# Kernel optimization log

Measured on AMD Instinct MI355X. Metric: run time of the kernel, lower is better.

## Reference

```python
import jax, jax.numpy as jnp
import numpy as np

B, L, D, H = 4, 2048, 1024, 16
NEG = 1e7


def pos_encodings(length, d_model, dtype):
    d_half = d_model // 2
    pos = jnp.arange(length, dtype=dtype)
    freqs = jnp.arange(d_half, dtype=dtype)
    periods = 1.0 / (10000.0 ** (freqs / d_half))
    ang = pos[:, None] * periods[None, :]          # [L, D/2]
    # interleave: even cols = sin, odd cols = cos
    return jnp.stack([jnp.sin(ang), jnp.cos(ang)], axis=-1).reshape(length, d_model)


def setup_inputs() -> dict:
    key = jax.random.key(0)
    ks = jax.random.split(key, 12)
    s = 1.0 / np.sqrt(D)
    return {
        "q": jax.random.normal(ks[0], (B, L, D), jnp.float32),
        "k": jax.random.normal(ks[1], (B, L, D), jnp.float32),
        "v": jax.random.normal(ks[2], (B, L, D), jnp.float32),
        "padding": jnp.zeros((B, L), dtype=bool),
        "Wq": jax.random.normal(ks[3], (D, D), jnp.float32) * s,
        "bq": jax.random.normal(ks[4], (D,), jnp.float32) * s,
        "Wk": jax.random.normal(ks[5], (D, D), jnp.float32) * s,
        "bk": jax.random.normal(ks[6], (D,), jnp.float32) * s,
        "Wv": jax.random.normal(ks[7], (D, D), jnp.float32) * s,
        "bv": jax.random.normal(ks[8], (D,), jnp.float32) * s,
        "Wo": jax.random.normal(ks[9], (D, D), jnp.float32) * s,
        "bo": jax.random.normal(ks[10], (D,), jnp.float32) * s,
    }


def reference(q, k, v, padding, Wq, bq, Wk, bk, Wv, bv, Wo, bo):
    dtype = q.dtype
    d_head = D // H
    pe = pos_encodings(L, D, dtype)                # cache_index = 0

    qp = (q + pe) @ Wq + bq                        # [B, L, D]
    kp = (k + pe) @ Wk + bk
    vp = v @ Wv + bv

    # ... l (h d) -> ... h l d
    def split_heads(x):
        return x.reshape(B, L, H, d_head).transpose(0, 2, 1, 3)

    qh, kh, vh = split_heads(qp), split_heads(kp), split_heads(vp)

    scores = jnp.einsum('bhqd,bhkd->bhqk', qh, kh) * (d_head ** -0.5)

    causal = jnp.triu(jnp.ones((L, L), dtype=bool), k=1)       # [L, L]
    mask = padding[:, None, None, :] | causal                  # [B, 1, L, L]
    scores = scores - mask.astype(scores.dtype) * NEG

    out = jnp.einsum('bhqk,bhkd->bhqd', jax.nn.softmax(scores, axis=-1), vh)
    out = out.transpose(0, 2, 1, 3).reshape(B, L, D)           # ... h l d -> ... l (h d)
    return out @ Wo + bo
```

## Files before the change

### kernel.cpp

```cpp
#include <hip/hip_runtime.h>
#include <hip/hip_bf16.h>


typedef __bf16 bf16_t;
typedef bf16_t bf16x8 __attribute__((ext_vector_type(8)));
typedef bf16_t bf16x4 __attribute__((ext_vector_type(4)));
typedef float  f32x4  __attribute__((ext_vector_type(4)));

#define MFMA_16x16x32(a, b, c) __builtin_amdgcn_mfma_f32_16x16x32_bf16((a), (b), (c), 0, 0, 0)

constexpr int Lc = 2048, Dc = 1024;
constexpr int Mc = 8192;
#define QSCALE 0.18033688011112042f

__device__ __forceinline__ void gload16(const void* g, void* l) {
  __builtin_amdgcn_global_load_lds(
      (const __attribute__((address_space(1))) void*)g,
      (__attribute__((address_space(3))) void*)l, 16, 0, 0);
}

template <bool DO_V>
__global__ __launch_bounds__(256)
void qkv_prep_kernel(const float* __restrict__ q, const float* __restrict__ k,
                     const float* __restrict__ v, bf16_t* __restrict__ Aq,
                     bf16_t* __restrict__ Ak, bf16_t* __restrict__ Av) {
  int id  = blockIdx.x * 256 + threadIdx.x;
  int row = id >> 7;
  int c   = (id & 127) * 8;
  int pos = row & (Lc - 1);
  float period = __expf(-(float)(c >> 1) * 0.017988946039015984f);
  const float ratio = 0.98217189f;
  float pe8[8];
#pragma unroll
  for (int j = 0; j < 4; ++j) {
    float rev = ((float)pos * period) * 0.15915494309189535f;
    float rf = rev - floorf(rev);
    pe8[2 * j]     = __builtin_amdgcn_sinf(rf);
    pe8[2 * j + 1] = __builtin_amdgcn_cosf(rf);
    period *= ratio;
  }
  size_t off = (size_t)row * Dc + c;
  f32x4 q0 = *(const f32x4*)&q[off], q1 = *(const f32x4*)&q[off + 4];
  f32x4 k0 = *(const f32x4*)&k[off], k1 = *(const f32x4*)&k[off + 4];
  bf16x8 aq, ak;
#pragma unroll
  for (int e = 0; e < 4; ++e) {
    aq[e]     = (bf16_t)(q0[e] + pe8[e]);
    aq[4 + e] = (bf16_t)(q1[e] + pe8[4 + e]);
    ak[e]     = (bf16_t)(k0[e] + pe8[e]);
    ak[4 + e] = (bf16_t)(k1[e] + pe8[4 + e]);
  }
  *(bf16x8*)&Aq[off] = aq;
  *(bf16x8*)&Ak[off] = ak;
  if (DO_V) {
    f32x4 v0 = *(const f32x4*)&v[off], v1 = *(const f32x4*)&v[off + 4];
    bf16x8 av;
#pragma unroll
    for (int e = 0; e < 4; ++e) { av[e] = (bf16_t)v0[e]; av[4 + e] = (bf16_t)v1[e]; }
    *(bf16x8*)&Av[off] = av;
  }
}

__device__ __forceinline__ void w_prep_body(const float* W, bf16_t* Wt, int tid, int blk) {
  __shared__ float tile[64][65];
  int k0 = (blk >> 4) * 64, n0 = (blk & 15) * 64;
  int tc = tid & 63, tr = tid >> 6;
#pragma unroll
  for (int j = 0; j < 16; ++j) {
    int r = j * 4 + tr;
    tile[r][tc] = W[(size_t)(k0 + r) * Dc + n0 + tc];
  }
  __syncthreads();
#pragma unroll
  for (int j = 0; j < 16; ++j) {
    int r = j * 4 + tr;
    Wt[(size_t)(n0 + r) * Dc + k0 + tc] = (bf16_t)tile[tc][r];
  }
}

__global__ __launch_bounds__(256)
void w_prep_kernel(const float* __restrict__ W, bf16_t* __restrict__ Wt) {
  w_prep_body(W, Wt, threadIdx.x, blockIdx.x);
}

__global__ __launch_bounds__(256)
void w_prep4_kernel(const float* __restrict__ W0, const float* __restrict__ W1,
                    const float* __restrict__ W2, const float* __restrict__ W3,
                    bf16_t* __restrict__ Wt) {
  int sel = blockIdx.x >> 8;
  const float* W = (sel == 0) ? W0 : (sel == 1) ? W1 : (sel == 2) ? W2 : W3;
  w_prep_body(W, Wt + (size_t)sel * Dc * Dc, threadIdx.x, blockIdx.x & 255);
}

template <int TMODE, typename OutT, int SEGS>
__global__ __launch_bounds__(512, 4)
void gemm_db_kernel(const bf16_t* __restrict__ A0, const bf16_t* __restrict__ A1,
                    const bf16_t* __restrict__ A2,
                    const bf16_t* __restrict__ W0, const bf16_t* __restrict__ W1,
                    const bf16_t* __restrict__ W2,
                    const float* __restrict__ b0, const float* __restrict__ b1,
                    const float* __restrict__ b2,
                    OutT* __restrict__ C0, OutT* __restrict__ C1,
                    OutT* __restrict__ C2,
                    float s0, float s1, float s2) {
  constexpr int K = 1024, N = 1024, LDS_T = 136;
  __shared__ bf16_t smem[32768];
  int bid = blockIdx.x;
  int seg = (SEGS >= 2) ? (bid >> 9) : 0;
  bid &= 511;
  const bf16_t* A    = (seg == 0) ? A0 : (seg == 1) ? A1 : A2;
  const bf16_t* Wt   = (seg == 0) ? W0 : (seg == 1) ? W1 : W2;
  const float*  bias = (seg == 0) ? b0 : (seg == 1) ? b1 : b2;
  OutT*         C    = (seg == 0) ? C0 : (seg == 1) ? C1 : C2;
  float scale        = (seg == 0) ? s0 : (seg == 1) ? s1 : s2;
  bool dotrans       = (TMODE == 1) || (TMODE == 2 && seg == 2);
  int xcd = bid & 7, slot = bid >> 3;
  int m0 = (xcd * 8 + (slot >> 3)) * 128;
  int n0 = (slot & 7) * 128;
  int t = threadIdx.x, lane = t & 63, w = t >> 6;
  int l16 = lane & 15, lq = lane >> 4;
  int wm = (w >> 1) * 32, wn = (w & 1) * 64;
  int srow = lane >> 3;
  int scol = ((lane & 7) ^ srow) << 3;
  int swz = l16 & 7;
  f32x4 acc[2][4] = {};

  auto STAGE = [&](int c, int k0) {
    bf16_t* Ash = &smem[c * 16384];
    bf16_t* Bsh = Ash + 8192;
#pragma unroll
    for (int j = 0; j < 2; ++j) {
      int r8 = (w * 2 + j) * 8;
      gload16(&A[(size_t)(m0 + r8 + srow) * K + k0 + scol], &Ash[r8 * 64]);
      gload16(&Wt[(size_t)(n0 + r8 + srow) * K + k0 + scol], &Bsh[r8 * 64]);
    }
  };

  STAGE(0, 0);
  int c = 0;
#pragma unroll 1
  for (int ti = 0; ti < 16; ++ti) {
    if (ti < 15) {
      STAGE(c ^ 1, (ti + 1) * 64);
      asm volatile("s_waitcnt vmcnt(4)" ::: "memory");
    } else {
      asm volatile("s_waitcnt vmcnt(0)" ::: "memory");
    }
    __builtin_amdgcn_s_barrier();
    const bf16_t* Ash = &smem[c * 16384];
    const bf16_t* Bsh = Ash + 8192;
#pragma unroll
    for (int ks = 0; ks < 2; ++ks) {
      bf16x8 af[2], bfr[4];
#pragma unroll
      for (int mt = 0; mt < 2; ++mt)
        af[mt] = *(const bf16x8*)&Ash[(wm + mt * 16 + l16) * 64 + (((ks * 4 + lq) ^ swz) << 3)];
#pragma unroll
      for (int nt = 0; nt < 4; ++nt)
        bfr[nt] = *(const bf16x8*)&Bsh[(wn + nt * 16 + l16) * 64 + (((ks * 4 + lq) ^ swz) << 3)];
#pragma unroll
      for (int mt = 0; mt < 2; ++mt)
#pragma unroll
        for (int nt = 0; nt < 4; ++nt)
          acc[mt][nt] = MFMA_16x16x32(af[mt], bfr[nt], acc[mt][nt]);
    }
    __builtin_amdgcn_s_barrier();
    c ^= 1;
  }

  if (dotrans) {
    bf16_t* sT = smem;
#pragma unroll
    for (int nt = 0; nt < 4; ++nt) {
      float bv = bias[n0 + wn + nt * 16 + l16];
#pragma unroll
      for (int mt = 0; mt < 2; ++mt) {
        bf16x4 p4;
#pragma unroll
        for (int r = 0; r < 4; ++r) p4[r] = (bf16_t)(acc[mt][nt][r] + bv);
        *(bf16x4*)&sT[(wn + nt * 16 + l16) * LDS_T + wm + mt * 16 + lq * 4] = p4;
      }
    }
    __syncthreads();
    int b = m0 >> 11, kp0 = m0 & (Lc - 1);
#pragma unroll
    for (int i = 0; i < 4; ++i) {
      int cidx = t + i * 512;
      int coln = cidx >> 4, cc = (cidx & 15) * 8;
      *(bf16x8*)&((bf16_t*)C)[((size_t)b * 1024 + n0 + coln) * (size_t)Lc + kp0 + cc] =
          *(const bf16x8*)&sT[coln * LDS_T + cc];
    }
  } else {
#pragma unroll
    for (int nt = 0; nt < 4; ++nt) {
      float bv = bias[n0 + wn + nt * 16 + l16];
#pragma unroll
      for (int mt = 0; mt < 2; ++mt) {
        int row = m0 + wm + mt * 16 + lq * 4;
        int col = n0 + wn + nt * 16 + l16;
#pragma unroll
        for (int r = 0; r < 4; ++r)
          C[(size_t)(row + r) * N + col] = (OutT)((acc[mt][nt][r] + bv) * scale);
      }
    }
  }
}

__global__ __launch_bounds__(512, 4)
void gemm_af32_kernel(const float* __restrict__ A, const bf16_t* __restrict__ Wt,
                      const float* __restrict__ bias, bf16_t* __restrict__ C) {
  constexpr int K = 1024, LDS_T = 136;
  __shared__ bf16_t smem[17408];
  bf16_t* Ash = smem;
  bf16_t* Bsh = smem + 8192;
  int bid = blockIdx.x;
  int xcd = bid & 7, slot = bid >> 3;
  int m0 = (xcd * 8 + (slot >> 3)) * 128;
  int n0 = (slot & 7) * 128;
  int t = threadIdx.x, lane = t & 63, w = t >> 6;
  int l16 = lane & 15, lq = lane >> 4;
  int wm = (w >> 1) * 32, wn = (w & 1) * 64;
  int srow = lane >> 3;
  int scol = ((lane & 7) ^ srow) << 3;
  int swz = l16 & 7;
  f32x4 acc[2][4] = {};

  for (int k0 = 0; k0 < K; k0 += 64) {
#pragma unroll
    for (int i = 0; i < 2; ++i) {
      int id = t + i * 512;
      int row = id >> 3, cc = (id & 7) * 8;
      f32x4 a0 = *(const f32x4*)&A[(size_t)(m0 + row) * K + k0 + cc];
      f32x4 a1 = *(const f32x4*)&A[(size_t)(m0 + row) * K + k0 + cc + 4];
      bf16x8 ah;
#pragma unroll
      for (int e = 0; e < 4; ++e) { ah[e] = (bf16_t)a0[e]; ah[4 + e] = (bf16_t)a1[e]; }
      *(bf16x8*)&Ash[row * 64 + (((cc >> 3) ^ (row & 7)) << 3)] = ah;
    }
#pragma unroll
    for (int j = 0; j < 2; ++j) {
      int r8 = (w * 2 + j) * 8;
      gload16(&Wt[(size_t)(n0 + r8 + srow) * K + k0 + scol], &Bsh[r8 * 64]);
    }
    __syncthreads();
#pragma unroll
    for (int ks = 0; ks < 2; ++ks) {
      bf16x8 af[2], bfr[4];
#pragma unroll
      for (int mt = 0; mt < 2; ++mt)
        af[mt] = *(const bf16x8*)&Ash[(wm + mt * 16 + l16) * 64 + (((ks * 4 + lq) ^ swz) << 3)];
#pragma unroll
      for (int nt = 0; nt < 4; ++nt)
        bfr[nt] = *(const bf16x8*)&Bsh[(wn + nt * 16 + l16) * 64 + (((ks * 4 + lq) ^ swz) << 3)];
#pragma unroll
      for (int mt = 0; mt < 2; ++mt)
#pragma unroll
        for (int nt = 0; nt < 4; ++nt)
          acc[mt][nt] = MFMA_16x16x32(af[mt], bfr[nt], acc[mt][nt]);
    }
    __syncthreads();
  }

  bf16_t* sT = smem;
#pragma unroll
  for (int nt = 0; nt < 4; ++nt) {
    float bv = bias[n0 + wn + nt * 16 + l16];
#pragma unroll
    for (int mt = 0; mt < 2; ++mt) {
      bf16x4 p4;
#pragma unroll
      for (int r = 0; r < 4; ++r) p4[r] = (bf16_t)(acc[mt][nt][r] + bv);
      *(bf16x4*)&sT[(wn + nt * 16 + l16) * LDS_T + wm + mt * 16 + lq * 4] = p4;
    }
  }
  __syncthreads();
  int b = m0 >> 11, kp0 = m0 & (Lc - 1);
#pragma unroll
  for (int i = 0; i < 4; ++i) {
    int cidx = t + i * 512;
    int coln = cidx >> 4, cc = (cidx & 15) * 8;
    *(bf16x8*)&C[((size_t)b * 1024 + n0 + coln) * (size_t)Lc + kp0 + cc] =
        *(const bf16x8*)&sT[coln * LDS_T + cc];
  }
}

__global__ __launch_bounds__(256, 4)
void attn_kernel(const bf16_t* __restrict__ Qp, const bf16_t* __restrict__ Kp,
                 const bf16_t* __restrict__ VpT, bf16_t* __restrict__ O) {
  __shared__ bf16_t Ks[2][4096];
  __shared__ bf16_t Vt[2][4096];
  __shared__ bf16_t Ps[4096];
  int bid = blockIdx.x;
  int xcd = bid & 7, slot = bid >> 3;
  int bh = xcd * 8 + (slot >> 4);
  int px = slot & 15;
  int b = bh >> 4, h = bh & 15;
  int t = threadIdx.x, lane = t & 63, w = t >> 6;
  int l16 = lane & 15, lq = lane >> 4;
  int srow = lane >> 3;
  int scol = ((lane & 7) ^ srow) << 3;
  int swz = l16 & 7;
  const size_t base  = ((size_t)b * Lc) * Dc + h * 64;
  const size_t vbase = ((size_t)b * 1024 + h * 64) * (size_t)Lc;

  bf16x8 ones;
#pragma unroll
  for (int e = 0; e < 8; ++e) ones[e] = (bf16_t)1.0f;

  auto STAGE = [&](int cc, int kt) {
    int kbase = kt * 64;
#pragma unroll
    for (int j = 0; j < 2; ++j) {
      int r8 = (w * 2 + j) * 8;
      int row = r8 + srow;
      gload16(&Kp[base + (size_t)(kbase + row) * Dc + scol], &Ks[cc][r8 * 64]);
      gload16(&VpT[vbase + (size_t)row * Lc + kbase + scol], &Vt[cc][r8 * 64]);
    }
  };

#pragma unroll 1
  for (int phase = 0; phase < 2; ++phase) {
    int qt = phase ? 31 - px : px;
    int q0 = qt * 64;

    bf16x8 aq[2];
#pragma unroll
    for (int kd = 0; kd < 2; ++kd)
      aq[kd] = *(const bf16x8*)&Qp[base + (size_t)(q0 + w * 16 + l16) * Dc + kd * 32 + lq * 8];

    f32x4 oacc[4] = {};
    f32x4 lacc = {};
    int qrow = q0 + w * 16 + l16;

    STAGE(0, 0);
    int c = 0;
#pragma unroll 1
    for (int kt = 0; kt <= qt; ++kt) {
      if (kt < qt) {
        STAGE(c ^ 1, kt + 1);
        asm volatile("s_waitcnt vmcnt(4)" ::: "memory");
      } else {
        asm volatile("s_waitcnt vmcnt(0)" ::: "memory");
      }
      __builtin_amdgcn_s_barrier();

      int kbase = kt * 64;
      f32x4 sacc[4] = {};
#pragma unroll
      for (int ks = 0; ks < 2; ++ks) {
        bf16x8 bk[4];
#pragma unroll
        for (int nt = 0; nt < 4; ++nt)
          bk[nt] = *(const bf16x8*)&Ks[c][(nt * 16 + l16) * 64 + (((ks * 4 + lq) ^ swz) << 3)];
#pragma unroll
        for (int nt = 0; nt < 4; ++nt)
          sacc[nt] = MFMA_16x16x32(bk[nt], aq[ks], sacc[nt]);
      }

      if (kt == qt) {
#pragma unroll
        for (int nt = 0; nt < 4; ++nt)
#pragma unroll
          for (int r = 0; r < 4; ++r)
            if (kbase + nt * 16 + lq * 4 + r > qrow) sacc[nt][r] = -1.0e7f;
      }

#pragma unroll
      for (int nt = 0; nt < 4; ++nt) {
        bf16x4 p4;
#pragma unroll
        for (int r = 0; r < 4; ++r) p4[r] = (bf16_t)exp2f(sacc[nt][r]);
        int k4 = nt * 4 + lq;
        *(bf16x4*)&Ps[(w * 16 + l16) * 64 + (((k4 >> 1) ^ swz) << 3) + ((k4 & 1) << 2)] = p4;
      }

#pragma unroll
      for (int ks = 0; ks < 2; ++ks) {
        bf16x8 ap = *(const bf16x8*)&Ps[(w * 16 + l16) * 64 + (((ks * 4 + lq) ^ swz) << 3)];
        lacc = MFMA_16x16x32(ap, ones, lacc);
        bf16x8 bv[4];
#pragma unroll
        for (int nt = 0; nt < 4; ++nt)
          bv[nt] = *(const bf16x8*)&Vt[c][(nt * 16 + l16) * 64 + (((ks * 4 + lq) ^ swz) << 3)];
#pragma unroll
        for (int nt = 0; nt < 4; ++nt)
          oacc[nt] = MFMA_16x16x32(ap, bv[nt], oacc[nt]);
      }
      __builtin_amdgcn_s_barrier();
      c ^= 1;
    }

#pragma unroll
    for (int r = 0; r < 4; ++r) {
      float inv = __builtin_amdgcn_rcpf(lacc[r]);
      int row = q0 + w * 16 + lq * 4 + r;
#pragma unroll
      for (int nt = 0; nt < 4; ++nt)
        O[base + (size_t)row * Dc + nt * 16 + l16] = (bf16_t)(oacc[nt][r] * inv);
    }
  }
}

extern "C" void kernel_launch(void* const* d_in, const int* in_sizes, int n_in,
                              void* d_out, int out_size, void* d_ws, size_t ws_size,
                              hipStream_t stream) {
  (void)in_sizes; (void)n_in; (void)out_size;
  const float* q  = (const float*)d_in[0];
  const float* k  = (const float*)d_in[1];
  const float* v  = (const float*)d_in[2];
  const float* Wq = (const float*)d_in[4];
  const float* bq = (const float*)d_in[5];
  const float* Wk = (const float*)d_in[6];
  const float* bk = (const float*)d_in[7];
  const float* Wv = (const float*)d_in[8];
  const float* bv = (const float*)d_in[9];
  const float* Wo = (const float*)d_in[10];
  const float* bo = (const float*)d_in[11];
  float* out = (float*)d_out;

  char* ws = (char*)d_ws;
  constexpr size_t WT_B  = (size_t)Dc * Dc * 2;
  constexpr size_t MAT_B = (size_t)Mc * Dc * 2;
  constexpr size_t WSZ   = (size_t)Dc * Dc;

  if (ws_size >= 4 * WT_B + 6 * MAT_B) {
    bf16_t* WT  = (bf16_t*)(ws);
    bf16_t* Aq  = (bf16_t*)(ws + 4 * WT_B);
    bf16_t* Ak  = (bf16_t*)(ws + 4 * WT_B + 1 * MAT_B);
    bf16_t* Av  = (bf16_t*)(ws + 4 * WT_B + 2 * MAT_B);
    bf16_t* Qp  = (bf16_t*)(ws + 4 * WT_B + 3 * MAT_B);
    bf16_t* Kp  = (bf16_t*)(ws + 4 * WT_B + 4 * MAT_B);
    bf16_t* VpT = (bf16_t*)(ws + 4 * WT_B + 5 * MAT_B);
    bf16_t* Ob  = Qp;

    qkv_prep_kernel<true><<<4096, 256, 0, stream>>>(q, k, v, Aq, Ak, Av);
    w_prep4_kernel<<<1024, 256, 0, stream>>>(Wq, Wk, Wv, Wo, WT);
    gemm_db_kernel<2, bf16_t, 3><<<1536, 512, 0, stream>>>(
        Aq, Ak, Av, WT, WT + WSZ, WT + 2 * WSZ, bq, bk, bv,
        Qp, Kp, VpT, QSCALE, 1.0f, 1.0f);
    attn_kernel<<<1024, 256, 0, stream>>>(Qp, Kp, VpT, Ob);
    gemm_db_kernel<0, float, 1><<<512, 512, 0, stream>>>(
        Ob, Ob, Ob, WT + 3 * WSZ, WT + 3 * WSZ, WT + 3 * WSZ, bo, bo, bo,
        out, out, out, 1.0f, 1.0f, 1.0f);
  } else if (ws_size >= 4 * WT_B + 5 * MAT_B) {
    bf16_t* WT  = (bf16_t*)(ws);
    bf16_t* Aq  = (bf16_t*)(ws + 4 * WT_B);
    bf16_t* Ak  = (bf16_t*)(ws + 4 * WT_B + 1 * MAT_B);
    bf16_t* Av  = (bf16_t*)(ws + 4 * WT_B + 2 * MAT_B);
    bf16_t* Qp  = (bf16_t*)(ws + 4 * WT_B + 3 * MAT_B);
    bf16_t* Kp  = (bf16_t*)(ws + 4 * WT_B + 4 * MAT_B);
    bf16_t* VpT = Aq;
    bf16_t* Ob  = Qp;

    qkv_prep_kernel<true><<<4096, 256, 0, stream>>>(q, k, v, Aq, Ak, Av);
    w_prep4_kernel<<<1024, 256, 0, stream>>>(Wq, Wk, Wv, Wo, WT);
    gemm_db_kernel<0, bf16_t, 2><<<1024, 512, 0, stream>>>(
        Aq, Ak, Ak, WT, WT + WSZ, WT + WSZ, bq, bk, bk,
        Qp, Kp, Kp, QSCALE, 1.0f, 1.0f);
    gemm_db_kernel<1, bf16_t, 1><<<512, 512, 0, stream>>>(
        Av, Av, Av, WT + 2 * WSZ, WT + 2 * WSZ, WT + 2 * WSZ, bv, bv, bv,
        VpT, VpT, VpT, 1.0f, 1.0f, 1.0f);
    attn_kernel<<<1024, 256, 0, stream>>>(Qp, Kp, VpT, Ob);
    gemm_db_kernel<0, float, 1><<<512, 512, 0, stream>>>(
        Ob, Ob, Ob, WT + 3 * WSZ, WT + 3 * WSZ, WT + 3 * WSZ, bo, bo, bo,
        out, out, out, 1.0f, 1.0f, 1.0f);
  } else {
    bf16_t* WT  = (bf16_t*)(ws);
    bf16_t* Aq  = (bf16_t*)(ws + WT_B);
    bf16_t* Ak  = (bf16_t*)(ws + WT_B + 1 * MAT_B);
    bf16_t* Qp  = (bf16_t*)(ws + WT_B + 2 * MAT_B);
    bf16_t* Kp  = Aq;
    bf16_t* VpT = Ak;
    bf16_t* Ob  = Qp;

    qkv_prep_kernel<false><<<4096, 256, 0, stream>>>(q, k, nullptr, Aq, Ak, nullptr);

    w_prep_kernel<<<256, 256, 0, stream>>>(Wq, WT);
    gemm_db_kernel<0, bf16_t, 1><<<512, 512, 0, stream>>>(
        Aq, Aq, Aq, WT, WT, WT, bq, bq, bq, Qp, Qp, Qp, QSCALE, QSCALE, QSCALE);

    w_prep_kernel<<<256, 256, 0, stream>>>(Wk, WT);
    gemm_db_kernel<0, bf16_t, 1><<<512, 512, 0, stream>>>(
        Ak, Ak, Ak, WT, WT, WT, bk, bk, bk, Kp, Kp, Kp, 1.0f, 1.0f, 1.0f);

    w_prep_kernel<<<256, 256, 0, stream>>>(Wv, WT);
    gemm_af32_kernel<<<512, 512, 0, stream>>>(v, WT, bv, VpT);

    attn_kernel<<<1024, 256, 0, stream>>>(Qp, Kp, VpT, Ob);

    w_prep_kernel<<<256, 256, 0, stream>>>(Wo, WT);
    gemm_db_kernel<0, float, 1><<<512, 512, 0, stream>>>(
        Ob, Ob, Ob, WT, WT, WT, bo, bo, bo, out, out, out, 1.0f, 1.0f, 1.0f);
  }
}
```

Before: 312.0 us.

## Rewrite attention with 32x32 MFMA, register P via lane shuffles, fuse prep kernels

The attention kernel moves from 16x16x32 to 32x32x16 MFMA tiles. Each of two waves now owns 32 query rows, and the softmax probabilities are rearranged between the half-waves with a cross-lane shuffle instead of a round trip through shared memory, so the Ps buffer goes away. Block size drops to 128 threads, and each thread issues twice as many staging loads per tile. Separately, the activation-prep and weight-transpose kernels are merged into one launch to save a kernel launch, at the cost of fewer waves per block and larger accumulator register use in attention.

Result: slower. 324.7 us (+4.1%).

```diff
diff --git a/kernel.cpp b/kernel.cpp
--- a/kernel.cpp
+++ b/kernel.cpp
@@ -6,8 +6,10 @@
 typedef bf16_t bf16x8 __attribute__((ext_vector_type(8)));
 typedef bf16_t bf16x4 __attribute__((ext_vector_type(4)));
 typedef float  f32x4  __attribute__((ext_vector_type(4)));
+typedef float  f32x16 __attribute__((ext_vector_type(16)));
 
 #define MFMA_16x16x32(a, b, c) __builtin_amdgcn_mfma_f32_16x16x32_bf16((a), (b), (c), 0, 0, 0)
+#define MFMA_32x32x16(a, b, c) __builtin_amdgcn_mfma_f32_32x32x16_bf16((a), (b), (c), 0, 0, 0)
 
 constexpr int Lc = 2048, Dc = 1024;
 constexpr int Mc = 8192;
@@ -20,11 +22,9 @@
 }
 
 template <bool DO_V>
-__global__ __launch_bounds__(256)
-void qkv_prep_kernel(const float* __restrict__ q, const float* __restrict__ k,
-                     const float* __restrict__ v, bf16_t* __restrict__ Aq,
-                     bf16_t* __restrict__ Ak, bf16_t* __restrict__ Av) {
-  int id  = blockIdx.x * 256 + threadIdx.x;
+__device__ __forceinline__ void qkv_prep_body(
+    const float* q, const float* k, const float* v,
+    bf16_t* Aq, bf16_t* Ak, bf16_t* Av, int id) {
   int row = id >> 7;
   int c   = (id & 127) * 8;
   int pos = row & (Lc - 1);
@@ -61,6 +61,14 @@
   }
 }
 
+template <bool DO_V>
+__global__ __launch_bounds__(256)
+void qkv_prep_kernel(const float* __restrict__ q, const float* __restrict__ k,
+                     const float* __restrict__ v, bf16_t* __restrict__ Aq,
+                     bf16_t* __restrict__ Ak, bf16_t* __restrict__ Av) {
+  qkv_prep_body<DO_V>(q, k, v, Aq, Ak, Av, blockIdx.x * 256 + threadIdx.x);
+}
+
 __device__ __forceinline__ void w_prep_body(const float* W, bf16_t* Wt, int tid, int blk) {
   __shared__ float tile[64][65];
   int k0 = (blk >> 4) * 64, n0 = (blk & 15) * 64;
@@ -84,12 +92,20 @@
 }
 
 __global__ __launch_bounds__(256)
-void w_prep4_kernel(const float* __restrict__ W0, const float* __restrict__ W1,
-                    const float* __restrict__ W2, const float* __restrict__ W3,
-                    bf16_t* __restrict__ Wt) {
-  int sel = blockIdx.x >> 8;
-  const float* W = (sel == 0) ? W0 : (sel == 1) ? W1 : (sel == 2) ? W2 : W3;
-  w_prep_body(W, Wt + (size_t)sel * Dc * Dc, threadIdx.x, blockIdx.x & 255);
+void prep_fused_kernel(const float* __restrict__ q, const float* __restrict__ k,
+                       const float* __restrict__ v, bf16_t* __restrict__ Aq,
+                       bf16_t* __restrict__ Ak, bf16_t* __restrict__ Av,
+                       const float* __restrict__ W0, const float* __restrict__ W1,
+                       const float* __restrict__ W2, const float* __restrict__ W3,
+                       bf16_t* __restrict__ Wt) {
+  if (blockIdx.x >= 4096) {
+    int bb = blockIdx.x - 4096;
+    int sel = bb >> 8;
+    const float* W = (sel == 0) ? W0 : (sel == 1) ? W1 : (sel == 2) ? W2 : W3;
+    w_prep_body(W, Wt + (size_t)sel * Dc * Dc, threadIdx.x, bb & 255);
+    return;
+  }
+  qkv_prep_body<true>(q, k, v, Aq, Ak, Av, blockIdx.x * 256 + threadIdx.x);
 }
 
 template <int TMODE, typename OutT, int SEGS>
@@ -284,22 +300,20 @@
   }
 }
 
-__global__ __launch_bounds__(256, 4)
+__global__ __launch_bounds__(128, 2)
 void attn_kernel(const bf16_t* __restrict__ Qp, const bf16_t* __restrict__ Kp,
                  const bf16_t* __restrict__ VpT, bf16_t* __restrict__ O) {
   __shared__ bf16_t Ks[2][4096];
   __shared__ bf16_t Vt[2][4096];
-  __shared__ bf16_t Ps[4096];
   int bid = blockIdx.x;
   int xcd = bid & 7, slot = bid >> 3;
   int bh = xcd * 8 + (slot >> 4);
   int px = slot & 15;
   int b = bh >> 4, h = bh & 15;
   int t = threadIdx.x, lane = t & 63, w = t >> 6;
-  int l16 = lane & 15, lq = lane >> 4;
+  int l32 = lane & 31, hi = lane >> 5;
   int srow = lane >> 3;
   int scol = ((lane & 7) ^ srow) << 3;
-  int swz = l16 & 7;
   const size_t base  = ((size_t)b * Lc) * Dc + h * 64;
   const size_t vbase = ((size_t)b * 1024 + h * 64) * (size_t)Lc;
 
@@ -310,8 +324,8 @@
   auto STAGE = [&](int cc, int kt) {
     int kbase = kt * 64;
 #pragma unroll
-    for (int j = 0; j < 2; ++j) {
-      int r8 = (w * 2 + j) * 8;
+    for (int j = 0; j < 4; ++j) {
+      int r8 = (w * 4 + j) * 8;
       int row = r8 + srow;
       gload16(&Kp[base + (size_t)(kbase + row) * Dc + scol], &Ks[cc][r8 * 64]);
       gload16(&VpT[vbase + (size_t)row * Lc + kbase + scol], &Vt[cc][r8 * 64]);
@@ -322,15 +336,15 @@
   for (int phase = 0; phase < 2; ++phase) {
     int qt = phase ? 31 - px : px;
     int q0 = qt * 64;
-
-    bf16x8 aq[2];
-#pragma unroll
-    for (int kd = 0; kd < 2; ++kd)
-      aq[kd] = *(const bf16x8*)&Qp[base + (size_t)(q0 + w * 16 + l16) * Dc + kd * 32 + lq * 8];
-
-    f32x4 oacc[4] = {};
-    f32x4 lacc = {};
-    int qrow = q0 + w * 16 + l16;
+    int qrow = q0 + w * 32 + l32;
+
+    bf16x8 qf[4];
+#pragma unroll
+    for (int ds = 0; ds < 4; ++ds)
+      qf[ds] = *(const bf16x8*)&Qp[base + (size_t)qrow * Dc + ds * 16 + hi * 8];
+
+    f32x16 oacc[2] = {};
+    f32x16 lacc = {};
 
     STAGE(0, 0);
     int c = 0;
@@ -338,65 +352,82 @@
     for (int kt = 0; kt <= qt; ++kt) {
       if (kt < qt) {
         STAGE(c ^ 1, kt + 1);
-        asm volatile("s_waitcnt vmcnt(4)" ::: "memory");
+        asm volatile("s_waitcnt vmcnt(8)" ::: "memory");
       } else {
         asm volatile("s_waitcnt vmcnt(0)" ::: "memory");
       }
       __builtin_amdgcn_s_barrier();
 
+      f32x16 sacc[2] = {};
+#pragma unroll
+      for (int t32 = 0; t32 < 2; ++t32) {
+        int row = t32 * 32 + l32;
+        int rsw = (row & 7);
+#pragma unroll
+        for (int ds = 0; ds < 4; ++ds) {
+          bf16x8 kf = *(const bf16x8*)&Ks[c][row * 64 + (((ds * 2 + hi) ^ rsw) << 3)];
+          sacc[t32] = MFMA_32x32x16(kf, qf[ds], sacc[t32]);
+        }
+      }
+
       int kbase = kt * 64;
-      f32x4 sacc[4] = {};
-#pragma unroll
-      for (int ks = 0; ks < 2; ++ks) {
-        bf16x8 bk[4];
-#pragma unroll
-        for (int nt = 0; nt < 4; ++nt)
-          bk[nt] = *(const bf16x8*)&Ks[c][(nt * 16 + l16) * 64 + (((ks * 4 + lq) ^ swz) << 3)];
-#pragma unroll
-        for (int nt = 0; nt < 4; ++nt)
-          sacc[nt] = MFMA_16x16x32(bk[nt], aq[ks], sacc[nt]);
-      }
-
       if (kt == qt) {
 #pragma unroll
-        for (int nt = 0; nt < 4; ++nt)
-#pragma unroll
-          for (int r = 0; r < 4; ++r)
-            if (kbase + nt * 16 + lq * 4 + r > qrow) sacc[nt][r] = -1.0e7f;
-      }
-
-#pragma unroll
-      for (int nt = 0; nt < 4; ++nt) {
-        bf16x4 p4;
-#pragma unroll
-        for (int r = 0; r < 4; ++r) p4[r] = (bf16_t)exp2f(sacc[nt][r]);
-        int k4 = nt * 4 + lq;
-        *(bf16x4*)&Ps[(w * 16 + l16) * 64 + (((k4 >> 1) ^ swz) << 3) + ((k4 & 1) << 2)] = p4;
-      }
-
-#pragma unroll
-      for (int ks = 0; ks < 2; ++ks) {
-        bf16x8 ap = *(const bf16x8*)&Ps[(w * 16 + l16) * 64 + (((ks * 4 + lq) ^ swz) << 3)];
-        lacc = MFMA_16x16x32(ap, ones, lacc);
-        bf16x8 bv[4];
-#pragma unroll
-        for (int nt = 0; nt < 4; ++nt)
-          bv[nt] = *(const bf16x8*)&Vt[c][(nt * 16 + l16) * 64 + (((ks * 4 + lq) ^ swz) << 3)];
-#pragma unroll
-        for (int nt = 0; nt < 4; ++nt)
-          oacc[nt] = MFMA_16x16x32(ap, bv[nt], oacc[nt]);
+        for (int t32 = 0; t32 < 2; ++t32)
+#pragma unroll
+          for (int r = 0; r < 16; ++r) {
+            int kpos = kbase + t32 * 32 + (r & 3) + 8 * (r >> 2) + 4 * hi;
+            if (kpos > qrow) sacc[t32][r] = -1.0e7f;
+          }
+      }
+
+      bf16x4 pown[8];
+#pragma unroll
+      for (int t32 = 0; t32 < 2; ++t32)
+#pragma unroll
+        for (int g2 = 0; g2 < 4; ++g2) {
+          bf16x4 g;
+#pragma unroll
+          for (int r4 = 0; r4 < 4; ++r4) g[r4] = (bf16_t)exp2f(sacc[t32][g2 * 4 + r4]);
+          pown[t32 * 4 + g2] = g;
+        }
+
+      bf16x8 pa[4];
+#pragma unroll
+      for (int s = 0; s < 4; ++s) {
+        bf16x4 sendg = hi ? pown[2 * s] : pown[2 * s + 1];
+        unsigned long long sv = __builtin_bit_cast(unsigned long long, sendg);
+        unsigned long long rv = __shfl_xor(sv, 32);
+        bf16x4 rg = __builtin_bit_cast(bf16x4, rv);
+        bf16x4 glo = hi ? rg : pown[2 * s];
+        bf16x4 ghi = hi ? pown[2 * s + 1] : rg;
+        bf16x8 f;
+#pragma unroll
+        for (int e = 0; e < 4; ++e) { f[e] = glo[e]; f[4 + e] = ghi[e]; }
+        pa[s] = f;
+      }
+
+#pragma unroll
+      for (int s = 0; s < 4; ++s) {
+        lacc = MFMA_32x32x16(pa[s], ones, lacc);
+#pragma unroll
+        for (int dt = 0; dt < 2; ++dt) {
+          int row = dt * 32 + l32;
+          bf16x8 vf = *(const bf16x8*)&Vt[c][row * 64 + (((s * 2 + hi) ^ (row & 7)) << 3)];
+          oacc[dt] = MFMA_32x32x16(pa[s], vf, oacc[dt]);
+        }
       }
       __builtin_amdgcn_s_barrier();
       c ^= 1;
     }
 
 #pragma unroll
-    for (int r = 0; r < 4; ++r) {
+    for (int r = 0; r < 16; ++r) {
       float inv = __builtin_amdgcn_rcpf(lacc[r]);
-      int row = q0 + w * 16 + lq * 4 + r;
-#pragma unroll
-      for (int nt = 0; nt < 4; ++nt)
-        O[base + (size_t)row * Dc + nt * 16 + l16] = (bf16_t)(oacc[nt][r] * inv);
+      int qr = q0 + w * 32 + (r & 3) + 8 * (r >> 2) + 4 * hi;
+#pragma unroll
+      for (int dt = 0; dt < 2; ++dt)
+        O[base + (size_t)qr * Dc + dt * 32 + l32] = (bf16_t)(oacc[dt][r] * inv);
     }
   }
 }
@@ -433,12 +464,12 @@
     bf16_t* VpT = (bf16_t*)(ws + 4 * WT_B + 5 * MAT_B);
     bf16_t* Ob  = Qp;
 
-    qkv_prep_kernel<true><<<4096, 256, 0, stream>>>(q, k, v, Aq, Ak, Av);
-    w_prep4_kernel<<<1024, 256, 0, stream>>>(Wq, Wk, Wv, Wo, WT);
+    prep_fused_kernel<<<5120, 256, 0, stream>>>(q, k, v, Aq, Ak, Av,
+                                                Wq, Wk, Wv, Wo, WT);
     gemm_db_kernel<2, bf16_t, 3><<<1536, 512, 0, stream>>>(
         Aq, Ak, Av, WT, WT + WSZ, WT + 2 * WSZ, bq, bk, bv,
         Qp, Kp, VpT, QSCALE, 1.0f, 1.0f);
-    attn_kernel<<<1024, 256, 0, stream>>>(Qp, Kp, VpT, Ob);
+    attn_kernel<<<1024, 128, 0, stream>>>(Qp, Kp, VpT, Ob);
     gemm_db_kernel<0, float, 1><<<512, 512, 0, stream>>>(
         Ob, Ob, Ob, WT + 3 * WSZ, WT + 3 * WSZ, WT + 3 * WSZ, bo, bo, bo,
         out, out, out, 1.0f, 1.0f, 1.0f);
@@ -452,15 +483,15 @@
     bf16_t* VpT = Aq;
     bf16_t* Ob  = Qp;
 
-    qkv_prep_kernel<true><<<4096, 256, 0, stream>>>(q, k, v, Aq, Ak, Av);
-    w_prep4_kernel<<<1024, 256, 0, stream>>>(Wq, Wk, Wv, Wo, WT);
+    prep_fused_kernel<<<5120, 256, 0, stream>>>(q, k, v, Aq, Ak, Av,
+                                                Wq, Wk, Wv, Wo, WT);
     gemm_db_kernel<0, bf16_t, 2><<<1024, 512, 0, stream>>>(
         Aq, Ak, Ak, WT, WT + WSZ, WT + WSZ, bq, bk, bk,
         Qp, Kp, Kp, QSCALE, 1.0f, 1.0f);
     gemm_db_kernel<1, bf16_t, 1><<<512, 512, 0, stream>>>(
         Av, Av, Av, WT + 2 * WSZ, WT + 2 * WSZ, WT + 2 * WSZ, bv, bv, bv,
         VpT, VpT, VpT, 1.0f, 1.0f, 1.0f);
-    attn_kernel<<<1024, 256, 0, stream>>>(Qp, Kp, VpT, Ob);
+    attn_kernel<<<1024, 128, 0, stream>>>(Qp, Kp, VpT, Ob);
     gemm_db_kernel<0, float, 1><<<512, 512, 0, stream>>>(
         Ob, Ob, Ob, WT + 3 * WSZ, WT + 3 * WSZ, WT + 3 * WSZ, bo, bo, bo,
         out, out, out, 1.0f, 1.0f, 1.0f);
@@ -486,7 +517,7 @@
     w_prep_kernel<<<256, 256, 0, stream>>>(Wv, WT);
     gemm_af32_kernel<<<512, 512, 0, stream>>>(v, WT, bv, VpT);
 
-    attn_kernel<<<1024, 256, 0, stream>>>(Qp, Kp, VpT, Ob);
+    attn_kernel<<<1024, 128, 0, stream>>>(Qp, Kp, VpT, Ob);
 
     w_prep_kernel<<<256, 256, 0, stream>>>(Wo, WT);
     gemm_db_kernel<0, float, 1><<<512, 512, 0, stream>>>(
```
